# Performance work log

Hardware: AMD Instinct MI355X
Metric: run time of the kernel (lower is better)

Reference implementation:

```python
import jax, jax.numpy as jnp
import numpy as np

D_MODEL = 1024
MAX_LEN = 2048
ORDER = 2
BATCH = 4
SEQ = 2048


def setup_inputs() -> dict:
    key = jax.random.key(0)
    k1, k2, k3, k4 = jax.random.split(key, 4)
    x = jax.random.normal(k1, (BATCH, SEQ, D_MODEL), dtype=jnp.float32)
    # torch Linear(d, d*(order+1)): weight [out,in]; we store transposed [in,out]
    proj_w = jax.random.normal(k2, (D_MODEL, D_MODEL * (ORDER + 1)), dtype=jnp.float32) * (D_MODEL ** -0.5)
    proj_b = jax.random.normal(k3, (D_MODEL * (ORDER + 1),), dtype=jnp.float32) * 0.02
    filter_time = jax.random.normal(k4, (ORDER, 1, MAX_LEN, D_MODEL), dtype=jnp.float32) / (MAX_LEN ** 0.5)
    return {"x": x, "proj_w": proj_w, "proj_b": proj_b, "filter_time": filter_time}


def reference(x, proj_w, proj_b, filter_time):
    B, L, D = x.shape
    order, _, max_length, _ = filter_time.shape
    fft_size = 2 * max_length
    # projection -> [B, L, order+1, D]
    p = (jnp.einsum('bld,de->ble', x, proj_w) + proj_b).reshape(B, L, order + 1, D)
    v = p[:, :, 0, :]  # value stream [B, L, D]
    for stage in range(order):
        # zero-padding to fft_size is implicit via n=fft_size; real FFT is the
        # real-valued-optimized equivalent of fft->complex-mul->ifft.real
        vf = jnp.fft.rfft(v, n=fft_size, axis=1)                      # [B, fft/2+1, D]
        ff = jnp.fft.rfft(filter_time[stage], n=fft_size, axis=1)    # [1, fft/2+1, D]
        conv = jnp.fft.irfft(vf * ff, n=fft_size, axis=1)[:, :L, :]  # causal slice
        v = conv * p[:, :, stage + 1, :]                              # gate
    return v
```

## Files before the change

kernel.cpp:

```cpp
#include <hip/hip_runtime.h>
#include <hip/hip_bf16.h>

#define B_     4
#define L_     2048
#define D_     1024
#define MAXLEN 2048
#define N_     3072
#define K_     1024
#define KP     40

typedef __attribute__((ext_vector_type(8))) short short8;
typedef __attribute__((ext_vector_type(4))) short short4v;
typedef __attribute__((ext_vector_type(4))) float f32x4;

__device__ __forceinline__ short f2bf(float x) {
    return __builtin_bit_cast(short, (__bf16)x);
}
__device__ __forceinline__ float bf2f(short h) {
    return (float)__builtin_bit_cast(__bf16, h);
}

__global__ __launch_bounds__(256) void wsplit_kernel(
    const float* __restrict__ W, short* __restrict__ WtH, short* __restrict__ WtL)
{
    __shared__ float lds[64][65];
    const int n0 = blockIdx.x * 64;
    const int k0 = blockIdx.y * 64;
    const int t  = threadIdx.x;
    const int nc = t & 63;
#pragma unroll
    for (int i = 0; i < 16; ++i) {
        const int kr = i * 4 + (t >> 6);
        lds[kr][nc] = W[(size_t)(k0 + kr) * N_ + n0 + nc];
    }
    __syncthreads();
    const int kg = (t & 15) * 4;
#pragma unroll
    for (int r = 0; r < 4; ++r) {
        const int nr = (t >> 4) + r * 16;
        short4v hv, lv;
#pragma unroll
        for (int j = 0; j < 4; ++j) {
            const float x = lds[kg + j][nr];
            const short h = f2bf(x);
            hv[j] = h;
            lv[j] = f2bf(x - bf2f(h));
        }
        const size_t o = (size_t)(n0 + nr) * K_ + k0 + kg;
        *(short4v*)&WtH[o] = hv;
        *(short4v*)&WtL[o] = lv;
    }
}

__global__ __launch_bounds__(256) void gemm_mfma_kernel(
    const float* __restrict__ X, const short* __restrict__ WtH,
    const short* __restrict__ WtL, const float* __restrict__ bias,
    float* __restrict__ p0, float* __restrict__ p1, float* __restrict__ p2)
{
    __shared__ __align__(16) short Ah[128][KP];
    __shared__ __align__(16) short Al[128][KP];
    __shared__ __align__(16) short Bh[128][KP];
    __shared__ __align__(16) short Bl[128][KP];

    const int tid = threadIdx.x;
    const int m0 = blockIdx.y * 128;
    const int n0 = blockIdx.x * 128;

    const int lane = tid & 63;
    const int wave = tid >> 6;
    const int wr = wave >> 1;
    const int wc = wave & 1;
    const int fr = lane & 15;
    const int fq = lane >> 4;

    const int srow  = tid >> 1;
    const int shalf = (tid & 1) * 16;

    f32x4 acc[4][4];
#pragma unroll
    for (int m = 0; m < 4; ++m)
#pragma unroll
        for (int n = 0; n < 4; ++n) acc[m][n] = (f32x4){0.f, 0.f, 0.f, 0.f};

    const float* xp  = &X[(size_t)(m0 + srow) * K_ + shalf];
    const short* bhp = &WtH[(size_t)(n0 + srow) * K_ + shalf];
    const short* blp = &WtL[(size_t)(n0 + srow) * K_ + shalf];

    for (int k0 = 0; k0 < K_; k0 += 32) {
        float xv[16];
        *(float4*)&xv[0]  = *(const float4*)&xp[k0];
        *(float4*)&xv[4]  = *(const float4*)&xp[k0 + 4];
        *(float4*)&xv[8]  = *(const float4*)&xp[k0 + 8];
        *(float4*)&xv[12] = *(const float4*)&xp[k0 + 12];
        short8 ah[2], al[2];
#pragma unroll
        for (int g = 0; g < 2; ++g)
#pragma unroll
            for (int j = 0; j < 8; ++j) {
                const float x = xv[g * 8 + j];
                const short h = f2bf(x);
                ah[g][j] = h;
                al[g][j] = f2bf(x - bf2f(h));
            }
        *(short8*)&Ah[srow][shalf]     = ah[0];
        *(short8*)&Ah[srow][shalf + 8] = ah[1];
        *(short8*)&Al[srow][shalf]     = al[0];
        *(short8*)&Al[srow][shalf + 8] = al[1];
        *(short8*)&Bh[srow][shalf]     = *(const short8*)&bhp[k0];
        *(short8*)&Bh[srow][shalf + 8] = *(const short8*)&bhp[k0 + 8];
        *(short8*)&Bl[srow][shalf]     = *(const short8*)&blp[k0];
        *(short8*)&Bl[srow][shalf + 8] = *(const short8*)&blp[k0 + 8];
        __syncthreads();

        short8 aH[4], aL[4], bH[4], bL[4];
#pragma unroll
        for (int m = 0; m < 4; ++m) {
            aH[m] = *(const short8*)&Ah[wr * 64 + m * 16 + fr][fq * 8];
            aL[m] = *(const short8*)&Al[wr * 64 + m * 16 + fr][fq * 8];
        }
#pragma unroll
        for (int n = 0; n < 4; ++n) {
            bH[n] = *(const short8*)&Bh[wc * 64 + n * 16 + fr][fq * 8];
            bL[n] = *(const short8*)&Bl[wc * 64 + n * 16 + fr][fq * 8];
        }
#pragma unroll
        for (int m = 0; m < 4; ++m)
#pragma unroll
            for (int n = 0; n < 4; ++n) {
                acc[m][n] = __builtin_amdgcn_mfma_f32_16x16x32_bf16(aH[m], bH[n], acc[m][n], 0, 0, 0);
                acc[m][n] = __builtin_amdgcn_mfma_f32_16x16x32_bf16(aH[m], bL[n], acc[m][n], 0, 0, 0);
                acc[m][n] = __builtin_amdgcn_mfma_f32_16x16x32_bf16(aL[m], bH[n], acc[m][n], 0, 0, 0);
            }
        __syncthreads();
    }

    const int s = n0 >> 10;
    float* outp = (s == 0) ? p0 : ((s == 1) ? p1 : p2);
    const int csub = n0 & 1023;
#pragma unroll
    for (int n = 0; n < 4; ++n) {
        const int gcol = wc * 64 + n * 16 + fr;
        const float bv = bias[n0 + gcol];
        const int col = csub + gcol;
#pragma unroll
        for (int m = 0; m < 4; ++m) {
            const int rowb = m0 + wr * 64 + m * 16 + fq * 4;
#pragma unroll
            for (int j = 0; j < 4; ++j)
                outp[(size_t)(rowb + j) * D_ + col] = acc[m][n][j] + bv;
        }
    }
}

__global__ __launch_bounds__(512, 1) void conv_stage_kernel(
    const float* __restrict__ vin, const float* __restrict__ filt,
    const float* __restrict__ gate, float* __restrict__ vout)
{
    __shared__ float v_lds[64][128];
    __shared__ float f4[48][128][4];

    const int d0 = blockIdx.x * 128;
    const int yp = blockIdx.y;
    const int b  = blockIdx.z;
    const int tid = threadIdx.x;
    const int dl = tid & 127;
    const int rg = tid >> 7;
    const int r0 = rg * 32;

    const int sr = tid >> 5;
    const int sc = (tid & 31) * 4;
    const int fch = tid & 127;
    const int fq0 = tid >> 7;

    const float* vin_b = vin + (size_t)b * L_ * D_;

#define FWQ(i) fwq[((i) & 63) >> 2][(i) & 3]

    for (int half = 0; half < 2; ++half) {
        const int yt = (half == 0) ? yp : (15 - yp);
        const int l0 = yt * 128;
        const int ntiles = 2 * yt + 2;
        int c_cur = l0 % 192;

        __syncthreads();
        {
#pragma unroll
            for (int s = 0; s < 4; ++s) {
                const float4 q = *(const float4*)&vin_b[(size_t)(sr + 16*s) * D_ + d0 + sc];
                *(float4*)&v_lds[sr + 16*s][sc] = q;
            }
            const int base0 = l0 - 63;
#pragma unroll
            for (int s = 0; s < 12; ++s) {
                const int qr = fq0 + 4*s;
                int qsg = (c_cur >> 2) + qr; if (qsg >= 48) qsg -= 48;
                f32x4 q;
#pragma unroll
                for (int e = 0; e < 4; ++e) {
                    const int a = base0 + 4*qr + e;
                    float fv = 0.f;
                    if (a >= 0 && a < MAXLEN) fv = filt[(size_t)a * D_ + d0 + fch];
                    q[e] = fv;
                }
                *(f32x4*)&f4[qsg][fch][0] = q;
            }
        }
        __syncthreads();

        float4 pv[4];
        f32x4 pf4[4];
#pragma unroll
        for (int s = 0; s < 4; ++s)
            pv[s] = *(const float4*)&vin_b[(size_t)(64 + sr + 16*s) * D_ + d0 + sc];
        {
            const int base1 = l0 - 127;
#pragma unroll
            for (int s = 0; s < 4; ++s) {
                const int qr = fq0 + 4*s;
#pragma unroll
                for (int e = 0; e < 4; ++e) {
                    const int a = base1 + 4*qr + e;
                    float fv = 0.f;
                    if (a >= 0 && a < MAXLEN) fv = filt[(size_t)a * D_ + d0 + fch];
                    pf4[s][e] = fv;
                }
            }
        }

        float acc[32];
#pragma unroll
        for (int j = 0; j < 32; ++j) acc[j] = 0.f;

        for (int ti = 0; ti < ntiles; ++ti) {
            f32x4 fwq[16];
#pragma unroll
            for (int s2 = 0; s2 < 12; ++s2) {
                const int K = 48 + 4*s2;
                int x = c_cur + r0 + K; if (x >= 192) x -= 192;
                fwq[(K & 63) >> 2] = *(const f32x4*)&f4[x >> 2][dl][0];
            }
            float vv[2][4];
#pragma unroll
            for (int u = 0; u < 4; ++u) vv[0][u] = v_lds[u][dl];

#pragma unroll
            for (int si = 0; si < 16; ++si) {
                const int tb = 4 * si;
                if ((si & 3) == 0 && si < 12) {
                    const int g = si >> 2;
#pragma unroll
                    for (int s2 = 0; s2 < 4; ++s2) {
                        const int K = 32 - 16*g + 4*s2;
                        int x = c_cur + r0 + K; if (x >= 192) x -= 192;
                        fwq[(K & 63) >> 2] = *(const f32x4*)&f4[x >> 2][dl][0];
                    }
                }
                if (si < 15) {
#pragma unroll
                    for (int u = 0; u < 4; ++u)
                        vv[(si + 1) & 1][u] = v_lds[tb + 4 + u][dl];
                }
#pragma unroll
                for (int u = 0; u < 4; ++u)
#pragma unroll
                    for (int j = 0; j < 32; ++j)
                        acc[j] += vv[si & 1][u] * FWQ(63 - tb + j - u);
            }

            if (ti + 1 < ntiles) {
                int c_next = c_cur - 64; if (c_next < 0) c_next += 192;
                __syncthreads();
#pragma unroll
                for (int s = 0; s < 4; ++s)
                    *(float4*)&v_lds[sr + 16*s][sc] = pv[s];
#pragma unroll
                for (int s = 0; s < 4; ++s) {
                    const int qsg = (c_next >> 2) + fq0 + 4*s;
                    *(f32x4*)&f4[qsg][fch][0] = pf4[s];
                }
                __syncthreads();
                if (ti + 2 < ntiles) {
                    const int t0n = 64 * (ti + 2);
#pragma unroll
                    for (int s = 0; s < 4; ++s)
                        pv[s] = *(const float4*)&vin_b[(size_t)(t0n + sr + 16*s) * D_ + d0 + sc];
                    const int basen = l0 - t0n - 63;
#pragma unroll
                    for (int s = 0; s < 4; ++s) {
                        const int qr = fq0 + 4*s;
#pragma unroll
                        for (int e = 0; e < 4; ++e) {
                            const int a = basen + 4*qr + e;
                            float fv = 0.f;
                            if (a >= 0 && a < MAXLEN) fv = filt[(size_t)a * D_ + d0 + fch];
                            pf4[s][e] = fv;
                        }
                    }
                }
                c_cur = c_next;
            }
        }

        const size_t off = (size_t)b * L_ * D_ + (size_t)l0 * D_ + d0 + dl;
#pragma unroll
        for (int j = 0; j < 32; ++j) {
            const size_t idx = off + (size_t)(r0 + j) * D_;
            vout[idx] = acc[j] * gate[idx];
        }
    }
#undef FWQ
}

extern "C" void kernel_launch(void* const* d_in, const int* in_sizes, int n_in,
                              void* d_out, int out_size, void* d_ws, size_t ws_size,
                              hipStream_t stream) {
    const float* x  = (const float*)d_in[0];
    const float* w  = (const float*)d_in[1];
    const float* bb = (const float*)d_in[2];
    const float* ft = (const float*)d_in[3];
    float* out = (float*)d_out;

    float* p0 = (float*)d_ws;
    float* p1 = p0 + (size_t)B_ * L_ * D_;
    float* p2 = p1 + (size_t)B_ * L_ * D_;

    short* WtH = (short*)d_out;
    short* WtL = WtH + (size_t)N_ * K_;

    wsplit_kernel<<<dim3(N_ / 64, K_ / 64), 256, 0, stream>>>(w, WtH, WtL);

    gemm_mfma_kernel<<<dim3(N_ / 128, (B_ * L_) / 128), 256, 0, stream>>>(
        x, WtH, WtL, bb, p0, p1, p2);

    conv_stage_kernel<<<dim3(D_ / 128, 8, B_), 512, 0, stream>>>(
        p0, ft, p1, p1);

    conv_stage_kernel<<<dim3(D_ / 128, 8, B_), 512, 0, stream>>>(
        p1, ft + (size_t)MAXLEN * D_, p2, out);
}
```

Before: 794.2 us.

## Cut conv kernel register use to allow two blocks per CU

Raises launch bounds on the direct-convolution stage kernel to ask for two 512-thread blocks per CU. To fit, it shrinks the filter register window from 16 to 12 quads, loaded as a rolling window one quad per sub-step, and drops the register prefetch of the next v/filter tile, which is now loaded only after the barrier. The aim is to hide latency through extra resident waves instead of software prefetch. The risk is that global-load latency now sits exposed between barriers, and spills may appear if the compiler cannot meet the tighter register budget.

```diff
diff --git a/kernel.cpp b/kernel.cpp
--- a/kernel.cpp
+++ b/kernel.cpp
@@ -152,7 +152,7 @@
     }
 }
 
-__global__ __launch_bounds__(512, 1) void conv_stage_kernel(
+__global__ __launch_bounds__(512, 2) void conv_stage_kernel(
     const float* __restrict__ vin, const float* __restrict__ filt,
     const float* __restrict__ gate, float* __restrict__ vout)
 {
@@ -174,7 +174,7 @@
 
     const float* vin_b = vin + (size_t)b * L_ * D_;
 
-#define FWQ(i) fwq[((i) & 63) >> 2][(i) & 3]
+#define FWQ(i) fwq[((i) >> 2) % 12][(i) & 3]
 
     for (int half = 0; half < 2; ++half) {
         const int yt = (half == 0) ? yp : (15 - yp);
@@ -207,37 +207,19 @@
         }
         __syncthreads();
 
-        float4 pv[4];
-        f32x4 pf4[4];
-#pragma unroll
-        for (int s = 0; s < 4; ++s)
-            pv[s] = *(const float4*)&vin_b[(size_t)(64 + sr + 16*s) * D_ + d0 + sc];
-        {
-            const int base1 = l0 - 127;
-#pragma unroll
-            for (int s = 0; s < 4; ++s) {
-                const int qr = fq0 + 4*s;
-#pragma unroll
-                for (int e = 0; e < 4; ++e) {
-                    const int a = base1 + 4*qr + e;
-                    float fv = 0.f;
-                    if (a >= 0 && a < MAXLEN) fv = filt[(size_t)a * D_ + d0 + fch];
-                    pf4[s][e] = fv;
-                }
-            }
-        }
-
         float acc[32];
 #pragma unroll
         for (int j = 0; j < 32; ++j) acc[j] = 0.f;
 
         for (int ti = 0; ti < ntiles; ++ti) {
-            f32x4 fwq[16];
-#pragma unroll
-            for (int s2 = 0; s2 < 12; ++s2) {
-                const int K = 48 + 4*s2;
-                int x = c_cur + r0 + K; if (x >= 192) x -= 192;
-                fwq[(K & 63) >> 2] = *(const f32x4*)&f4[x >> 2][dl][0];
+            int base4 = (c_cur + r0) >> 2;
+            if (base4 >= 48) base4 -= 48;
+
+            f32x4 fwq[12];
+#pragma unroll
+            for (int q = 15; q <= 23; ++q) {
+                int x4 = base4 + q; if (x4 >= 48) x4 -= 48;
+                fwq[q % 12] = *(const f32x4*)&f4[x4][dl][0];
             }
             float vv[2][4];
 #pragma unroll
@@ -246,16 +228,10 @@
 #pragma unroll
             for (int si = 0; si < 16; ++si) {
                 const int tb = 4 * si;
-                if ((si & 3) == 0 && si < 12) {
-                    const int g = si >> 2;
-#pragma unroll
-                    for (int s2 = 0; s2 < 4; ++s2) {
-                        const int K = 32 - 16*g + 4*s2;
-                        int x = c_cur + r0 + K; if (x >= 192) x -= 192;
-                        fwq[(K & 63) >> 2] = *(const f32x4*)&f4[x >> 2][dl][0];
-                    }
-                }
                 if (si < 15) {
+                    const int q = 14 - si;
+                    int x4 = base4 + q; if (x4 >= 48) x4 -= 48;
+                    fwq[q % 12] = *(const f32x4*)&f4[x4][dl][0];
 #pragma unroll
                     for (int u = 0; u < 4; ++u)
                         vv[(si + 1) & 1][u] = v_lds[tb + 4 + u][dl];
@@ -269,34 +245,34 @@
 
             if (ti + 1 < ntiles) {
                 int c_next = c_cur - 64; if (c_next < 0) c_next += 192;
+                const int t0n = 64 * (ti + 1);
+                const int basen = l0 - t0n - 63;
                 __syncthreads();
+                float4 tv[4];
+                f32x4 tf[4];
 #pragma unroll
                 for (int s = 0; s < 4; ++s)
-                    *(float4*)&v_lds[sr + 16*s][sc] = pv[s];
+                    tv[s] = *(const float4*)&vin_b[(size_t)(t0n + sr + 16*s) * D_ + d0 + sc];
+#pragma unroll
+                for (int s = 0; s < 4; ++s) {
+                    const int qr = fq0 + 4*s;
+#pragma unroll
+                    for (int e = 0; e < 4; ++e) {
+                        const int a = basen + 4*qr + e;
+                        float fv = 0.f;
+                        if (a >= 0 && a < MAXLEN) fv = filt[(size_t)a * D_ + d0 + fch];
+                        tf[s][e] = fv;
+                    }
+                }
+#pragma unroll
+                for (int s = 0; s < 4; ++s)
+                    *(float4*)&v_lds[sr + 16*s][sc] = tv[s];
 #pragma unroll
                 for (int s = 0; s < 4; ++s) {
                     const int qsg = (c_next >> 2) + fq0 + 4*s;
-                    *(f32x4*)&f4[qsg][fch][0] = pf4[s];
+                    *(f32x4*)&f4[qsg][fch][0] = tf[s];
                 }
                 __syncthreads();
-                if (ti + 2 < ntiles) {
-                    const int t0n = 64 * (ti + 2);
-#pragma unroll
-                    for (int s = 0; s < 4; ++s)
-                        pv[s] = *(const float4*)&vin_b[(size_t)(t0n + sr + 16*s) * D_ + d0 + sc];
-                    const int basen = l0 - t0n - 63;
-#pragma unroll
-                    for (int s = 0; s < 4; ++s) {
-                        const int qr = fq0 + 4*s;
-#pragma unroll
-                        for (int e = 0; e < 4; ++e) {
-                            const int a = basen + 4*qr + e;
-                            float fv = 0.f;
-                            if (a >= 0 && a < MAXLEN) fv = filt[(size_t)a * D_ + d0 + fch];
-                            pf4[s][e] = fv;
-                        }
-                    }
-                }
                 c_cur = c_next;
             }
         }
```

Result: faster. 701.2 us (-11.7%).
